# Performance work log

Measured on AMD Instinct MI355X. Metric: run time of the kernel, lower is better.

Reference implementation:

```python
import jax, jax.numpy as jnp
import numpy as np

IN = (16, 16, 16)
OUT = (16, 16, 16)
RT = (8, 8, 8, 8, 8, 8)
RCP = 16
BATCH = 4096


def setup_inputs() -> dict:
    key = jax.random.key(0)
    ks = jax.random.split(key, 14)
    inp = {"x": jax.random.normal(ks[0], (BATCH, int(np.prod(IN))), dtype=jnp.float32)}
    # CP factors of the 6D Tucker core: (rank_tucker_i, rank_cp)
    for i in range(6):
        inp[f"c{i}"] = jax.random.normal(ks[1 + i], (RT[i], RCP), dtype=jnp.float32) * 0.1
    # Tucker factor matrices: out modes then in modes
    dims = list(OUT) + list(IN)
    for i in range(6):
        inp[f"f{i}"] = jax.random.normal(ks[7 + i], (dims[i], RT[i]), dtype=jnp.float32) * 0.1
    inp["bias"] = jnp.zeros((int(np.prod(OUT)),), dtype=jnp.float32)
    return inp


def reference(x, c0, c1, c2, c3, c4, c5, f0, f1, f2, f3, f4, f5, bias):
    # Reconstruct 6D core from its CP factors: (r0,r1,r2,r3,r4,r5)
    core = jnp.einsum('ir,jr,kr,lr,mr,nr->ijklmn', c0, c1, c2, c3, c4, c5)
    # Tucker reconstruction of full weight tensor: (o0,o1,o2,i0,i1,i2)
    W = jnp.einsum('ijklmn,ai,bj,ck,dl,em,fn->abcdef', core, f0, f1, f2, f3, f4, f5)
    x_reshape = x.reshape(-1, *IN)  # (N, i0, i1, i2)
    result = jnp.einsum('abcdef,ndef->nabc', W, x_reshape)  # (N, o0, o1, o2)
    y = result.reshape(-1, int(np.prod(OUT)))
    return y + bias
```

## Files before the change

kernel.cpp:

```cpp
#include <hip/hip_runtime.h>


typedef float f32x4 __attribute__((ext_vector_type(4)));

#define WPB 4

__global__ __launch_bounds__(256, 2)
void kruskal_fused(const float* __restrict__ x,
                   const float* __restrict__ c0, const float* __restrict__ c1,
                   const float* __restrict__ c2, const float* __restrict__ c3,
                   const float* __restrict__ c4, const float* __restrict__ c5,
                   const float* __restrict__ f0, const float* __restrict__ f1,
                   const float* __restrict__ f2, const float* __restrict__ f3,
                   const float* __restrict__ f4, const float* __restrict__ f5,
                   const float* __restrict__ bias,
                   float* __restrict__ out, int N)
{
    __shared__ __align__(16) float g3t[256];
    __shared__ __align__(16) float g4t[256];
    __shared__ __align__(16) float g5t[256];
    __shared__ __align__(16) float g0c[256];
    __shared__ __align__(16) float g1t[256];
    __shared__ __align__(16) float g2t[256];
    __shared__ __align__(16) float bsh[4096];

    const int tid = threadIdx.x;
    {
        const int i = tid >> 4, r = tid & 15;
        float a0 = 0.f, a1 = 0.f, a2 = 0.f, a3 = 0.f, a4 = 0.f, a5 = 0.f;
#pragma unroll
        for (int k = 0; k < 8; ++k) {
            a0 += f0[i * 8 + k] * c0[k * 16 + r];
            a1 += f1[i * 8 + k] * c1[k * 16 + r];
            a2 += f2[i * 8 + k] * c2[k * 16 + r];
            a3 += f3[i * 8 + k] * c3[k * 16 + r];
            a4 += f4[i * 8 + k] * c4[k * 16 + r];
            a5 += f5[i * 8 + k] * c5[k * 16 + r];
        }
        g0c[i * 16 + r] = a0;
        g1t[r * 16 + i] = a1;
        g2t[r * 16 + i] = a2;
        g3t[i * 16 + r] = a3;
        g4t[r * 16 + i] = a4;
        g5t[r * 16 + i] = a5;
    }
    {
        const f32x4* b4 = (const f32x4*)bias;
        f32x4* bs4 = (f32x4*)bsh;
#pragma unroll
        for (int j = 0; j < 4; ++j) bs4[j * 256 + tid] = b4[j * 256 + tid];
    }
    __syncthreads();

    const int lane = tid & 63, waveId = tid >> 6;
    const int eb  = lane >> 2;
    const int fcb = (lane & 3) * 4;

    const int n = blockIdx.x * WPB + waveId;
    if (n >= N) return;
    const float* xn = x + (size_t)n * 4096 + lane * 4;

    f32x4 t[16];
#pragma unroll
    for (int r = 0; r < 16; ++r) t[r] = f32x4{0.f, 0.f, 0.f, 0.f};

#define LOAD4(v, dbase)                                                       \
    v##0 = __builtin_nontemporal_load((const f32x4*)(xn + ((dbase) + 0) * 256)); \
    v##1 = __builtin_nontemporal_load((const f32x4*)(xn + ((dbase) + 1) * 256)); \
    v##2 = __builtin_nontemporal_load((const f32x4*)(xn + ((dbase) + 2) * 256)); \
    v##3 = __builtin_nontemporal_load((const f32x4*)(xn + ((dbase) + 3) * 256));

#define COMP1(xv, d)                                                          \
    {                                                                         \
        _Pragma("unroll")                                                     \
        for (int rq = 0; rq < 4; ++rq) {                                      \
            const f32x4 g3q = *(const f32x4*)&g3t[(d) * 16 + rq * 4];         \
            _Pragma("unroll")                                                 \
            for (int rr = 0; rr < 4; ++rr)                                    \
                t[rq * 4 + rr] += g3q[rr] * xv;                               \
        }                                                                     \
    }

#define COMP4(v, dbase)                                                       \
    COMP1(v##0, (dbase) + 0) COMP1(v##1, (dbase) + 1)                         \
    COMP1(v##2, (dbase) + 2) COMP1(v##3, (dbase) + 3)

    {
        f32x4 xa0, xa1, xa2, xa3, xb0, xb1, xb2, xb3;
        LOAD4(xa, 0)
        LOAD4(xb, 4)
        COMP4(xa, 0)
        LOAD4(xa, 8)
        COMP4(xb, 4)
        LOAD4(xb, 12)
        COMP4(xa, 8)
        COMP4(xb, 12)
    }
#undef LOAD4
#undef COMP1
#undef COMP4

    float s[16];
#pragma unroll
    for (int r = 0; r < 16; ++r) {
        const f32x4 w = (*(const f32x4*)&g5t[r * 16 + fcb]) * g4t[r * 16 + eb];
        s[r] = w.x * t[r].x + w.y * t[r].y + w.z * t[r].z + w.w * t[r].w;
    }

    float k8[8];
    {
        const bool b = lane & 1;
#pragma unroll
        for (int j = 0; j < 8; ++j) {
            const float snd = b ? s[2 * j] : s[2 * j + 1];
            const float prt = __shfl_xor(snd, 1, 64);
            const float kp  = b ? s[2 * j + 1] : s[2 * j];
            k8[j] = kp + prt;
        }
    }
    float k4[4];
    {
        const bool b = (lane >> 1) & 1;
#pragma unroll
        for (int j = 0; j < 4; ++j) {
            const float snd = b ? k8[2 * j] : k8[2 * j + 1];
            const float prt = __shfl_xor(snd, 2, 64);
            const float kp  = b ? k8[2 * j + 1] : k8[2 * j];
            k4[j] = kp + prt;
        }
    }
    float k2[2];
    {
        const bool b = (lane >> 2) & 1;
#pragma unroll
        for (int j = 0; j < 2; ++j) {
            const float snd = b ? k4[2 * j] : k4[2 * j + 1];
            const float prt = __shfl_xor(snd, 4, 64);
            const float kp  = b ? k4[2 * j + 1] : k4[2 * j];
            k2[j] = kp + prt;
        }
    }
    float k1;
    {
        const bool b = (lane >> 3) & 1;
        const float snd = b ? k2[0] : k2[1];
        const float prt = __shfl_xor(snd, 8, 64);
        const float kp  = b ? k2[1] : k2[0];
        k1 = kp + prt;
    }
    k1 += __shfl_xor(k1, 16, 64);
    k1 += __shfl_xor(k1, 32, 64);
    const int gbase = lane & 48;
#pragma unroll
    for (int r = 0; r < 16; ++r)
        s[r] = __shfl(k1, gbase | r, 64);

    __builtin_amdgcn_sched_barrier(0);

    f32x4 sw[16];
#pragma unroll
    for (int r = 0; r < 16; ++r)
        sw[r] = (*(const f32x4*)&g2t[r * 16 + fcb]) * (g1t[r * 16 + eb] * s[r]);

    float* on = out + (size_t)n * 4096;
#pragma unroll 2
    for (int a = 0; a < 16; ++a) {
        f32x4 acc = *(const f32x4*)&bsh[a * 256 + lane * 4];
#pragma unroll
        for (int rq = 0; rq < 4; ++rq) {
            const f32x4 g0q = *(const f32x4*)&g0c[a * 16 + rq * 4];
#pragma unroll
            for (int rr = 0; rr < 4; ++rr)
                acc += g0q[rr] * sw[rq * 4 + rr];
        }
        __builtin_nontemporal_store(
            acc, (f32x4*)(on + a * 256 + lane * 4));
    }
}

extern "C" void kernel_launch(void* const* d_in, const int* in_sizes, int n_in,
                              void* d_out, int out_size, void* d_ws, size_t ws_size,
                              hipStream_t stream) {
    const float* x  = (const float*)d_in[0];
    const float* c0 = (const float*)d_in[1];
    const float* c1 = (const float*)d_in[2];
    const float* c2 = (const float*)d_in[3];
    const float* c3 = (const float*)d_in[4];
    const float* c4 = (const float*)d_in[5];
    const float* c5 = (const float*)d_in[6];
    const float* f0 = (const float*)d_in[7];
    const float* f1 = (const float*)d_in[8];
    const float* f2 = (const float*)d_in[9];
    const float* f3 = (const float*)d_in[10];
    const float* f4 = (const float*)d_in[11];
    const float* f5 = (const float*)d_in[12];
    const float* bias = (const float*)d_in[13];
    float* out = (float*)d_out;
    (void)d_ws; (void)ws_size;

    const int N = in_sizes[0] / 4096;
    const int blocks = (N + WPB - 1) / WPB;

    kruskal_fused<<<dim3(blocks), dim3(256), 0, stream>>>(
        x, c0, c1, c2, c3, c4, c5, f0, f1, f2, f3, f4, f5, bias, out, N);
}
```

Measured before the change: 147.4 us.

## Precompute factor-core products in a separate kernel and shrink per-block LDS setup

Moves the six small factor×CP-core matrix products into a one-block prologue kernel that writes them to workspace, so each of the 1024 main blocks no longer recomputes them. The main kernel now stages only four of the matrices in a 4 KB LDS buffer and reads g3 and g0 straight from global memory through uniform loads. Bias is read from global memory instead of being copied into 16 KB of LDS. This cuts per-block setup and LDS footprint, which may allow more blocks per CU, at the cost of an extra kernel launch and global or scalar-cache loads in the inner loops.

```diff
diff --git a/kernel.cpp b/kernel.cpp
--- a/kernel.cpp
+++ b/kernel.cpp
@@ -4,51 +4,49 @@
 typedef float f32x4 __attribute__((ext_vector_type(4)));
 
 #define WPB 4
+
+
+__global__ __launch_bounds__(256)
+void kruskal_gmat(const float* __restrict__ c0, const float* __restrict__ c1,
+                  const float* __restrict__ c2, const float* __restrict__ c3,
+                  const float* __restrict__ c4, const float* __restrict__ c5,
+                  const float* __restrict__ f0, const float* __restrict__ f1,
+                  const float* __restrict__ f2, const float* __restrict__ f3,
+                  const float* __restrict__ f4, const float* __restrict__ f5,
+                  float* __restrict__ gw)
+{
+    const int t = threadIdx.x;
+    const int i = t >> 4, r = t & 15;
+    float a0 = 0.f, a1 = 0.f, a2 = 0.f, a3 = 0.f, a4 = 0.f, a5 = 0.f;
+#pragma unroll
+    for (int k = 0; k < 8; ++k) {
+        a0 += f0[i * 8 + k] * c0[k * 16 + r];
+        a1 += f1[i * 8 + k] * c1[k * 16 + r];
+        a2 += f2[i * 8 + k] * c2[k * 16 + r];
+        a3 += f3[i * 8 + k] * c3[k * 16 + r];
+        a4 += f4[i * 8 + k] * c4[k * 16 + r];
+        a5 += f5[i * 8 + k] * c5[k * 16 + r];
+    }
+    gw[         i * 16 + r] = a3;
+    gw[ 256 +   i * 16 + r] = a0;
+    gw[ 512 +   r * 16 + i] = a4;
+    gw[ 768 +   r * 16 + i] = a5;
+    gw[1024 +   r * 16 + i] = a1;
+    gw[1280 +   r * 16 + i] = a2;
+}
 
 __global__ __launch_bounds__(256, 2)
 void kruskal_fused(const float* __restrict__ x,
-                   const float* __restrict__ c0, const float* __restrict__ c1,
-                   const float* __restrict__ c2, const float* __restrict__ c3,
-                   const float* __restrict__ c4, const float* __restrict__ c5,
-                   const float* __restrict__ f0, const float* __restrict__ f1,
-                   const float* __restrict__ f2, const float* __restrict__ f3,
-                   const float* __restrict__ f4, const float* __restrict__ f5,
+                   const float* __restrict__ gw,
                    const float* __restrict__ bias,
                    float* __restrict__ out, int N)
 {
-    __shared__ __align__(16) float g3t[256];
-    __shared__ __align__(16) float g4t[256];
-    __shared__ __align__(16) float g5t[256];
-    __shared__ __align__(16) float g0c[256];
-    __shared__ __align__(16) float g1t[256];
-    __shared__ __align__(16) float g2t[256];
-    __shared__ __align__(16) float bsh[4096];
+    __shared__ __align__(16) float wlds[1024];
 
     const int tid = threadIdx.x;
     {
-        const int i = tid >> 4, r = tid & 15;
-        float a0 = 0.f, a1 = 0.f, a2 = 0.f, a3 = 0.f, a4 = 0.f, a5 = 0.f;
-#pragma unroll
-        for (int k = 0; k < 8; ++k) {
-            a0 += f0[i * 8 + k] * c0[k * 16 + r];
-            a1 += f1[i * 8 + k] * c1[k * 16 + r];
-            a2 += f2[i * 8 + k] * c2[k * 16 + r];
-            a3 += f3[i * 8 + k] * c3[k * 16 + r];
-            a4 += f4[i * 8 + k] * c4[k * 16 + r];
-            a5 += f5[i * 8 + k] * c5[k * 16 + r];
-        }
-        g0c[i * 16 + r] = a0;
-        g1t[r * 16 + i] = a1;
-        g2t[r * 16 + i] = a2;
-        g3t[i * 16 + r] = a3;
-        g4t[r * 16 + i] = a4;
-        g5t[r * 16 + i] = a5;
-    }
-    {
-        const f32x4* b4 = (const f32x4*)bias;
-        f32x4* bs4 = (f32x4*)bsh;
-#pragma unroll
-        for (int j = 0; j < 4; ++j) bs4[j * 256 + tid] = b4[j * 256 + tid];
+        const f32x4* src = (const f32x4*)(gw + 512);
+        ((f32x4*)wlds)[tid] = src[tid];
     }
     __syncthreads();
 
@@ -74,7 +72,7 @@
     {                                                                         \
         _Pragma("unroll")                                                     \
         for (int rq = 0; rq < 4; ++rq) {                                      \
-            const f32x4 g3q = *(const f32x4*)&g3t[(d) * 16 + rq * 4];         \
+            const f32x4 g3q = *(const f32x4*)(gw + (d) * 16 + rq * 4);        \
             _Pragma("unroll")                                                 \
             for (int rr = 0; rr < 4; ++rr)                                    \
                 t[rq * 4 + rr] += g3q[rr] * xv;                               \
@@ -100,10 +98,13 @@
 #undef COMP1
 #undef COMP4
 
+    __builtin_amdgcn_sched_barrier(0);
+
     float s[16];
 #pragma unroll
     for (int r = 0; r < 16; ++r) {
-        const f32x4 w = (*(const f32x4*)&g5t[r * 16 + fcb]) * g4t[r * 16 + eb];
+        const f32x4 w = (*(const f32x4*)&wlds[256 + r * 16 + fcb])
+                      * wlds[r * 16 + eb];
         s[r] = w.x * t[r].x + w.y * t[r].y + w.z * t[r].z + w.w * t[r].w;
     }
 
@@ -160,15 +161,16 @@
     f32x4 sw[16];
 #pragma unroll
     for (int r = 0; r < 16; ++r)
-        sw[r] = (*(const f32x4*)&g2t[r * 16 + fcb]) * (g1t[r * 16 + eb] * s[r]);
-
+        sw[r] = (*(const f32x4*)&wlds[768 + r * 16 + fcb])
+              * (wlds[512 + r * 16 + eb] * s[r]);
+    const float* bl = bias + lane * 4;
     float* on = out + (size_t)n * 4096;
 #pragma unroll 2
     for (int a = 0; a < 16; ++a) {
-        f32x4 acc = *(const f32x4*)&bsh[a * 256 + lane * 4];
+        f32x4 acc = *(const f32x4*)(bl + a * 256);
 #pragma unroll
         for (int rq = 0; rq < 4; ++rq) {
-            const f32x4 g0q = *(const f32x4*)&g0c[a * 16 + rq * 4];
+            const f32x4 g0q = *(const f32x4*)(gw + 256 + a * 16 + rq * 4);
 #pragma unroll
             for (int rr = 0; rr < 4; ++rr)
                 acc += g0q[rr] * sw[rq * 4 + rr];
@@ -196,11 +198,13 @@
     const float* f5 = (const float*)d_in[12];
     const float* bias = (const float*)d_in[13];
     float* out = (float*)d_out;
-    (void)d_ws; (void)ws_size;
+    float* gw  = (float*)d_ws;
 
     const int N = in_sizes[0] / 4096;
     const int blocks = (N + WPB - 1) / WPB;
 
+    kruskal_gmat<<<dim3(1), dim3(256), 0, stream>>>(
+        c0, c1, c2, c3, c4, c5, f0, f1, f2, f3, f4, f5, gw);
     kruskal_fused<<<dim3(blocks), dim3(256), 0, stream>>>(
-        x, c0, c1, c2, c3, c4, c5, f0, f1, f2, f3, f4, f5, bias, out, N);
+        x, gw, bias, out, N);
 }
```

New measurement: 145.5 us. About the same (-1.3%).
